# Kernel optimization log

Measured on AMD Instinct MI355X. Metric: run time of the kernel, lower is better.

The kernel has to match this reference:

```python
import jax, jax.numpy as jnp
import numpy as np

B, S, H, QKV, NH, MLP = 4, 2048, 512, 512, 8, 2048
HD = QKV // NH
EPS = 1e-6


def _layernorm(x):
    # LayerNorm over last dim, no affine, eps=1e-6
    mu = jnp.mean(x, axis=-1, keepdims=True)
    var = jnp.mean(jnp.square(x - mu), axis=-1, keepdims=True)
    return (x - mu) * jax.lax.rsqrt(var + EPS)


def setup_inputs() -> dict:
    key = jax.random.key(0)
    ks = jax.random.split(key, 8)
    sc_in = 1.0 / np.sqrt(H)
    sc_qkv = 1.0 / np.sqrt(QKV)
    sc_mlp = 1.0 / np.sqrt(MLP)
    return {
        "input": jax.random.normal(ks[0], (B, S, H), dtype=jnp.float32),
        "mask": jnp.ones((B, S), dtype=jnp.float32),
        "Wq": jax.random.normal(ks[1], (H, QKV), dtype=jnp.float32) * sc_in,
        "Wk": jax.random.normal(ks[2], (H, QKV), dtype=jnp.float32) * sc_in,
        "Wv": jax.random.normal(ks[3], (H, QKV), dtype=jnp.float32) * sc_in,
        "Wo": jax.random.normal(ks[4], (QKV, H), dtype=jnp.float32) * sc_qkv,
        "W1": jax.random.normal(ks[5], (H, MLP), dtype=jnp.float32) * sc_in,
        "W2": jax.random.normal(ks[6], (MLP, H), dtype=jnp.float32) * sc_mlp,
    }


def reference(input, mask, Wq, Wk, Wv, Wo, W1, W2):
    # pre-mask + pre-norm
    x = input * mask[..., None]
    x = _layernorm(x)
    # qkv projections, split heads: [B,S,QKV] -> [B,NH,S,HD]
    def heads(t):
        return t.reshape(B, S, NH, HD).transpose(0, 2, 1, 3)
    q = heads(x @ Wq) * (1.0 / np.sqrt(HD))
    k = heads(x @ Wk)
    v = heads(x @ Wv)
    logits = jnp.einsum("bhqd,bhkd->bhqk", q, k)  # [B,NH,S,S]
    amask = mask[:, None, :, None]  # 'b q -> b 1 q 1'
    logits = logits + (-100000.0) * (1.0 - amask)
    att = jax.nn.softmax(logits, axis=-1)
    out = jnp.einsum("bhqk,bhkd->bhqd", att, v)
    out = out.transpose(0, 2, 1, 3).reshape(B, S, QKV)
    x = input + out @ Wo  # residual
    x = x * mask[..., None]
    y = _layernorm(x)
    ffn = jax.nn.gelu(y @ W1, approximate=False) @ W2
    return ffn + x
```

## Files before the change

### kernel.cpp

```cpp
#include <hip/hip_runtime.h>
#include <hip/hip_bf16.h>
#include <cmath>

typedef __attribute__((ext_vector_type(8))) short bf16x8;
typedef __attribute__((ext_vector_type(4))) short u16x4;
typedef __attribute__((ext_vector_type(4))) float f32x4;
typedef __attribute__((ext_vector_type(16))) float f32x16;
typedef unsigned short u16;
typedef unsigned int u32;

#define B_ 4
#define S_ 2048
#define H_ 512
#define NH_ 8
#define HD_ 64
#define MLP_ 2048
#define M_ (B_*S_)
#define LOG2E 1.44269504088896340736f

__device__ __forceinline__ float bf2f(u16 u){ u32 v=((u32)u)<<16; float f; __builtin_memcpy(&f,&v,4); return f; }
__device__ __forceinline__ u16 f2bf(float f){ u32 u; __builtin_memcpy(&u,&f,4); u32 r=(u+0x7fffu+((u>>16)&1u))>>16; return (u16)r; }
__device__ __forceinline__ u32 pk2(float lo, float hi2){
  __hip_bfloat162 t = __float22bfloat162_rn(make_float2(lo, hi2));
  u32 r; __builtin_memcpy(&r, &t, 4); return r;
}

__device__ __forceinline__ float xhalf_add(float x){
  float a = x, b = x;
  asm volatile("v_permlane32_swap_b32 %0, %1" : "+v"(a), "+v"(b));
  return a + b;
}

__device__ __forceinline__ float gelu_fast(float x){
  float arg = 2.30221265f*x + 0.10295034f*x*x*x;
  arg = fminf(fmaxf(arg, -30.0f), 30.0f);
  float e = __builtin_amdgcn_exp2f(arg);
  return x * e * __builtin_amdgcn_rcpf(1.0f + e);
}

__device__ __forceinline__ void gl16(const u16* g, u16* l) {
  __builtin_amdgcn_global_load_lds((const __attribute__((address_space(1))) u32*)(g),
                                   (__attribute__((address_space(3))) u32*)(l), 16, 0, 0);
}

__device__ __forceinline__ void swz_mn(int* mt, int* nt) {
  int lin = blockIdx.x + 64*blockIdx.y;
  int xcd = lin & 7, idx = lin >> 3;
  *mt = xcd*8 + (idx & 7);
  *nt = idx >> 3;
}

__device__ __forceinline__ void gemm_core(
    const u16* __restrict__ A, const u16* __restrict__ Bt,
    int lda, int ldb, int nkt, int m0, int n0,
    u16* As, u16* Bs, f32x4 (&acc)[4][4])
{
  const int tid = threadIdx.x;
  const int lane = tid & 63;
  const int w = tid >> 6;
  const int lr = lane & 15;
  const int g  = lane >> 4;
  const int wr = w >> 1, wc = w & 1;

  const int sr = lane >> 3;
  const int scol = ((lane & 7) ^ sr) << 3;

  int aoff[2][4], boff[2][4];
#pragma unroll
  for (int m = 0; m < 4; ++m) {
    int ra = wr*64 + m*16 + lr;
    int rb = wc*64 + m*16 + lr;
#pragma unroll
    for (int kk = 0; kk < 2; ++kk) {
      aoff[kk][m] = ra*64 + (((kk*4+g) ^ (ra&7))<<3);
      boff[kk][m] = rb*64 + (((kk*4+g) ^ (rb&7))<<3);
    }
  }
  const u16* Ap = A + (size_t)m0*lda;
  const u16* Bp = Bt + (size_t)n0*ldb;

#pragma unroll
  for (int c = 0; c < 4; ++c) {
    gl16(Ap + (size_t)(w*32 + c*8 + sr)*lda + scol, As + w*2048 + c*512);
    gl16(Bp + (size_t)(w*32 + c*8 + sr)*ldb + scol, Bs + w*2048 + c*512);
  }

  for (int kt = 0; kt < nkt; ++kt) {
    const int cb = (kt & 1) * 8192;
    if (kt + 1 < nkt) {
      const int k0 = (kt + 1) << 6;
      const int nb = ((kt + 1) & 1) * 8192;
#pragma unroll
      for (int c = 0; c < 4; ++c) {
        gl16(Ap + (size_t)(w*32 + c*8 + sr)*lda + k0 + scol, As + nb + w*2048 + c*512);
        gl16(Bp + (size_t)(w*32 + c*8 + sr)*ldb + k0 + scol, Bs + nb + w*2048 + c*512);
      }
      asm volatile("s_waitcnt vmcnt(8)" ::: "memory");
    } else {
      asm volatile("s_waitcnt vmcnt(0)" ::: "memory");
    }
    __builtin_amdgcn_s_barrier();

#pragma unroll
    for (int kk = 0; kk < 2; ++kk) {
      bf16x8 af[4], bfr[4];
#pragma unroll
      for (int m = 0; m < 4; ++m) {
        af[m]  = *(const bf16x8*)(As + cb + aoff[kk][m]);
        bfr[m] = *(const bf16x8*)(Bs + cb + boff[kk][m]);
      }
#pragma unroll
      for (int m = 0; m < 4; ++m) {
#pragma unroll
        for (int n = 0; n < 4; ++n) {
          acc[m][n] = __builtin_amdgcn_mfma_f32_16x16x32_bf16(af[m], bfr[n], acc[m][n], 0, 0, 0);
        }
      }
    }
    __builtin_amdgcn_s_barrier();
  }
}

__device__ __forceinline__ void gemm_core64(
    const u16* __restrict__ A, const u16* __restrict__ Bt,
    int lda, int ldb, int nkt, int m0, int n0,
    u16* As, u16* Bs, f32x4 (&acc)[2][4])
{
  const int tid = threadIdx.x;
  const int lane = tid & 63;
  const int w = tid >> 6;
  const int lr = lane & 15;
  const int g  = lane >> 4;

  const int sr = lane >> 3;
  const int scol = ((lane & 7) ^ sr) << 3;

  int aoff[2][2], boff[2][4];
#pragma unroll
  for (int m = 0; m < 2; ++m) {
    int ra = w*32 + m*16 + lr;
#pragma unroll
    for (int kk = 0; kk < 2; ++kk) aoff[kk][m] = ra*64 + (((kk*4+g) ^ (ra&7))<<3);
  }
#pragma unroll
  for (int n = 0; n < 4; ++n) {
    int rb = n*16 + lr;
#pragma unroll
    for (int kk = 0; kk < 2; ++kk) boff[kk][n] = rb*64 + (((kk*4+g) ^ (rb&7))<<3);
  }
  const u16* Ap = A + (size_t)m0*lda;
  const u16* Bp = Bt + (size_t)n0*ldb;

#pragma unroll
  for (int c = 0; c < 4; ++c)
    gl16(Ap + (size_t)(w*32 + c*8 + sr)*lda + scol, As + w*2048 + c*512);
#pragma unroll
  for (int c = 0; c < 2; ++c)
    gl16(Bp + (size_t)(w*16 + c*8 + sr)*ldb + scol, Bs + w*1024 + c*512);

  for (int kt = 0; kt < nkt; ++kt) {
    const int cbA = (kt & 1) * 8192;
    const int cbB = (kt & 1) * 4096;
    if (kt + 1 < nkt) {
      const int k0 = (kt + 1) << 6;
      const int nbA = ((kt + 1) & 1) * 8192;
      const int nbB = ((kt + 1) & 1) * 4096;
#pragma unroll
      for (int c = 0; c < 4; ++c)
        gl16(Ap + (size_t)(w*32 + c*8 + sr)*lda + k0 + scol, As + nbA + w*2048 + c*512);
#pragma unroll
      for (int c = 0; c < 2; ++c)
        gl16(Bp + (size_t)(w*16 + c*8 + sr)*ldb + k0 + scol, Bs + nbB + w*1024 + c*512);
      asm volatile("s_waitcnt vmcnt(6)" ::: "memory");
    } else {
      asm volatile("s_waitcnt vmcnt(0)" ::: "memory");
    }
    __builtin_amdgcn_s_barrier();

#pragma unroll
    for (int kk = 0; kk < 2; ++kk) {
      bf16x8 af[2], bfr[4];
#pragma unroll
      for (int m = 0; m < 2; ++m) af[m] = *(const bf16x8*)(As + cbA + aoff[kk][m]);
#pragma unroll
      for (int n = 0; n < 4; ++n) bfr[n] = *(const bf16x8*)(Bs + cbB + boff[kk][n]);
#pragma unroll
      for (int m = 0; m < 2; ++m) {
#pragma unroll
        for (int n = 0; n < 4; ++n) {
          acc[m][n] = __builtin_amdgcn_mfma_f32_16x16x32_bf16(af[m], bfr[n], acc[m][n], 0, 0, 0);
        }
      }
    }
    __builtin_amdgcn_s_barrier();
  }
}

__global__ __launch_bounds__(256,2) void k_qkv(
    const u16* __restrict__ xn, const u16* __restrict__ wqt,
    const u16* __restrict__ wkt, const u16* __restrict__ wvt,
    u16* __restrict__ q, u16* __restrict__ k, u16* __restrict__ vt)
{
  __shared__ u16 As[2*128*64], Bs[2*128*64];
  int mt, nt; swz_mn(&mt, &nt);
  int m0 = mt*128;
  int sel = nt >> 2;
  int n0 = (nt & 3)*128;
  const u16* Bt = sel==0 ? wqt : (sel==1 ? wkt : wvt);
  f32x4 acc[4][4] = {};
  gemm_core(xn, Bt, H_, H_, H_/64, m0, n0, As, Bs, acc);
  const int lane = threadIdx.x&63, w = threadIdx.x>>6;
  const int lr = lane&15, g = lane>>4, wr = w>>1, wc = w&1;
  if (sel == 2) {
#pragma unroll
    for (int m=0;m<4;++m) {
#pragma unroll
      for (int n=0;n<4;++n) {
        int rowb = m0 + wr*64 + m*16 + g*4;
        int col  = n0 + wc*64 + n*16 + lr;
        int b = rowb >> 11, s = rowb & 2047;
        int h = col >> 6, d = col & 63;
        u16x4 t;
#pragma unroll
        for (int r=0;r<4;++r) t[r] = (short)f2bf(acc[m][n][r]);
        *(u16x4*)(vt + ((size_t)((b*NH_ + h)*HD_ + d))*S_ + s) = t;
      }
    }
  } else {
    u16* O = sel==0 ? q : k;
#pragma unroll
    for (int m=0;m<4;++m) {
#pragma unroll
      for (int n=0;n<4;++n) {
#pragma unroll
        for (int r=0;r<4;++r) {
          int row = m0 + wr*64 + m*16 + g*4 + r;
          int col = n0 + wc*64 + n*16 + lr;
          O[(size_t)row*H_ + col] = f2bf(acc[m][n][r]);
        }
      }
    }
  }
}

template<int EPI>
__global__ __launch_bounds__(256,2) void k_gemm(
    const u16* __restrict__ A, const u16* __restrict__ Bt, void* __restrict__ Ov,
    const void* __restrict__ aux, const float* __restrict__ maskv,
    int N, int K)
{
  __shared__ u16 As[2*128*64], Bs[2*128*64];
  int mt, nt; swz_mn(&mt, &nt);
  int m0 = mt*128, n0 = nt*128;
  f32x4 acc[4][4] = {};
  gemm_core(A, Bt, K, K, K>>6, m0, n0, As, Bs, acc);
  const int lane = threadIdx.x&63, w = threadIdx.x>>6;
  const int lr = lane&15, g = lane>>4, wr = w>>1, wc = w&1;
#pragma unroll
  for (int m=0;m<4;++m) {
#pragma unroll
    for (int n=0;n<4;++n) {
#pragma unroll
      for (int r=0;r<4;++r) {
        int row = m0 + wr*64 + m*16 + g*4 + r;
        int col = n0 + wc*64 + n*16 + lr;
        float val = acc[m][n][r];
        if (EPI == 1) {
          ((u16*)Ov)[(size_t)row*N + col] = f2bf(gelu_fast(val));
        }
      }
    }
  }
}

template<int EPI>
__global__ __launch_bounds__(256,3) void k_gemm64(
    const u16* __restrict__ A, const u16* __restrict__ Bt, void* __restrict__ Ov,
    const void* __restrict__ aux, const float* __restrict__ maskv,
    int N, int K)
{
  __shared__ u16 As[2*128*64], Bs[2*64*64];
  int mt, nt; swz_mn(&mt, &nt);
  int m0 = mt*128, n0 = nt*64;
  f32x4 acc[2][4] = {};
  gemm_core64(A, Bt, K, K, K>>6, m0, n0, As, Bs, acc);
  const int lane = threadIdx.x&63, w = threadIdx.x>>6;
  const int lr = lane&15, g = lane>>4;
#pragma unroll
  for (int m=0;m<2;++m) {
#pragma unroll
    for (int n=0;n<4;++n) {
#pragma unroll
      for (int r=0;r<4;++r) {
        int row = m0 + w*32 + m*16 + g*4 + r;
        int col = n0 + n*16 + lr;
        float val = acc[m][n][r];
        if (EPI == 2) {
          float mv = maskv[row];
          val = (((const float*)aux)[(size_t)row*N + col] + val)*mv;
          ((u16*)Ov)[(size_t)row*N + col] = f2bf(val);
        } else if (EPI == 3) {
          val += bf2f(((const u16*)aux)[(size_t)row*N + col]);
          ((float*)Ov)[(size_t)row*N + col] = val;
        }
      }
    }
  }
}

__global__ __launch_bounds__(256) void k_lnb(const u16* __restrict__ in,
    u16* __restrict__ out)
{
  int row = blockIdx.x*4 + (threadIdx.x>>6);
  int lane = threadIdx.x & 63;
  bf16x8 d = *(const bf16x8*)(in + (size_t)row*H_ + lane*8);
  float x[8]; float s = 0.f, s2 = 0.f;
#pragma unroll
  for (int j=0;j<8;++j){ x[j] = bf2f((u16)d[j]); s += x[j]; s2 += x[j]*x[j]; }
#pragma unroll
  for (int m=1;m<32;m<<=1){ s += __shfl_xor(s,m); s2 += __shfl_xor(s2,m); }
  s = xhalf_add(s); s2 = xhalf_add(s2);
  float mu = s*(1.0f/H_);
  float var = s2*(1.0f/H_) - mu*mu;
  float inv = rsqrtf(var + 1e-6f);
  bf16x8 o;
#pragma unroll
  for (int j=0;j<8;++j) o[j] = (short)f2bf((x[j]-mu)*inv);
  *(bf16x8*)(out + (size_t)row*H_ + lane*8) = o;
}

__global__ __launch_bounds__(256) void k_pre(
    const float* __restrict__ Wq, const float* __restrict__ Wk,
    const float* __restrict__ Wv, const float* __restrict__ Wo,
    const float* __restrict__ W1, const float* __restrict__ W2,
    u16* __restrict__ wqt, u16* __restrict__ wkt, u16* __restrict__ wvt,
    u16* __restrict__ wot, u16* __restrict__ w1t, u16* __restrict__ w2t,
    const float* __restrict__ input, const float* __restrict__ mask,
    u16* __restrict__ xn)
{
  __shared__ u16 t[32][33];
  const int id = blockIdx.x;
  const int tx = threadIdx.x & 31, ty = threadIdx.x >> 5;

  if (id < 1024) {
    int z = id >> 8, tt = id & 255;
    const float* src = z==0?Wq : z==1?Wk : z==2?Wv : Wo;
    u16* dst = z==0?wqt : z==1?wkt : z==2?wvt : wot;
    float sc = (z==0) ? 0.125f*LOG2E : 1.0f;
    int c0 = (tt & 15)*32, r0 = (tt >> 4)*32;
#pragma unroll
    for (int i=0;i<32;i+=8) t[ty+i][tx] = f2bf(src[(size_t)(r0+ty+i)*512 + c0+tx]*sc);
    __syncthreads();
#pragma unroll
    for (int i=0;i<32;i+=8) dst[(size_t)(c0+ty+i)*512 + r0+tx] = t[tx][ty+i];
  } else if (id < 3072) {
    int z = (id-1024) >> 10, tt = (id-1024) & 1023;
    const float* src = z ? W2 : W1;
    u16* dst = z ? w2t : w1t;
    int R = z ? 2048 : 512;
    int C = z ? 512 : 2048;
    int a = tt & 63, bq = tt >> 6;
    int c0 = (z ? bq : a)*32;
    int r0 = (z ? a : bq)*32;
#pragma unroll
    for (int i=0;i<32;i+=8) t[ty+i][tx] = f2bf(src[(size_t)(r0+ty+i)*C + c0+tx]);
    __syncthreads();
#pragma unroll
    for (int i=0;i<32;i+=8) dst[(size_t)(c0+ty+i)*R + r0+tx] = t[tx][ty+i];
  } else {
    int row = (id-3072)*4 + (threadIdx.x>>6);
    int lane = threadIdx.x & 63;
    const f32x4* p = (const f32x4*)(input + (size_t)row*H_ + lane*8);
    f32x4 a = p[0], b = p[1];
    float mv = mask[row];
    float x[8]; float s = 0.f, s2 = 0.f;
#pragma unroll
    for (int j=0;j<4;++j){ x[j] = a[j]*mv; x[4+j] = b[j]*mv; }
#pragma unroll
    for (int j=0;j<8;++j){ s += x[j]; s2 += x[j]*x[j]; }
#pragma unroll
    for (int m=1;m<32;m<<=1){ s += __shfl_xor(s,m); s2 += __shfl_xor(s2,m); }
    s = xhalf_add(s); s2 = xhalf_add(s2);
    float mu = s*(1.0f/H_);
    float var = s2*(1.0f/H_) - mu*mu;
    float inv = rsqrtf(var + 1e-6f);
    bf16x8 o;
#pragma unroll
    for (int j=0;j<8;++j) o[j] = (short)f2bf((x[j]-mu)*inv);
    *(bf16x8*)(xn + (size_t)row*H_ + lane*8) = o;
  }
}

__global__ __launch_bounds__(256) void k_attn(
    const u16* __restrict__ q, const u16* __restrict__ kmat,
    const u16* __restrict__ vt, const float* __restrict__ mask,
    u16* __restrict__ o)
{
  __shared__ u16 Ks[2][64*64];
  __shared__ u16 Vs[2][64*64];
  __shared__ float bias[S_];
  __shared__ float lsums[4][32];

  const int tid = threadIdx.x;
  const int lane = tid & 63;
  const int w = tid >> 6;
  const int l31 = lane & 31;
  const int hi = lane >> 5;
  const int bh = blockIdx.y, b = bh >> 3, h = bh & 7;
  const int q0 = blockIdx.x * 128;

  const int sr = lane >> 3;
  const int sl = (lane & 7) ^ (sr & 7);
  const u16* ks0 = kmat + (size_t)(b*S_ + w*16 + sr)*H_ + h*HD_ + sl*8;
  const u16* ks1 = ks0 + (size_t)8*H_;
  const u16* vs0 = vt + ((size_t)bh*HD_ + w*16 + sr)*S_ + sl*8;
  const u16* vs1 = vs0 + (size_t)8*S_;

  {
    u16* kd = &Ks[0][0] + w*1024;
    u16* vd = &Vs[0][0] + w*1024;
    gl16(ks0, kd); gl16(ks1, kd + 512);
    gl16(vs0, vd); gl16(vs1, vd + 512);
  }

  for (int j = tid; j < S_; j += 256) bias[j] = -144269.5f * (1.0f - mask[b*S_ + j]);

  bf16x8 qf[4];
  {
    const u16* qp = q + (size_t)(b*S_ + q0 + w*32 + l31)*H_ + h*HD_ + hi*8;
#pragma unroll
    for (int ds = 0; ds < 4; ++ds) qf[ds] = *(const bf16x8*)(qp + ds*16);
  }

  f32x16 po0 = {}, po1 = {};
  float mreg = -1e30f, lsum = 0.f;

  __syncthreads();

  for (int jt = 0; jt < 32; ++jt) {
    const int buf = jt & 1;
    if (jt < 31) {
      const int j0 = (jt + 1) * 64;
      u16* kd = &Ks[buf ^ 1][0] + w*1024;
      u16* vd = &Vs[buf ^ 1][0] + w*1024;
      gl16(ks0 + (size_t)j0*H_, kd); gl16(ks1 + (size_t)j0*H_, kd + 512);
      gl16(vs0 + j0, vd);            gl16(vs1 + j0, vd + 512);
      asm volatile("s_waitcnt vmcnt(4)" ::: "memory");
    } else {
      asm volatile("s_waitcnt vmcnt(0)" ::: "memory");
    }
    __builtin_amdgcn_s_barrier();

    const u16* kt  = &Ks[buf][0];
    const u16* vtl = &Vs[buf][0];

    f32x16 s0, s1;
    const float* bp = &bias[jt*64 + hi*4];
#pragma unroll
    for (int kb = 0; kb < 2; ++kb) {
      f32x16 acc;
#pragma unroll
      for (int g2 = 0; g2 < 4; ++g2) {
        f32x4 b4 = *(const f32x4*)(bp + kb*32 + g2*8);
        acc[g2*4+0] = b4[0]; acc[g2*4+1] = b4[1];
        acc[g2*4+2] = b4[2]; acc[g2*4+3] = b4[3];
      }
      const int key = kb*32 + l31;
      const u16* kr = kt + key*64;
      __builtin_amdgcn_s_setprio(1);
#pragma unroll
      for (int ds = 0; ds < 4; ++ds) {
        bf16x8 kf = *(const bf16x8*)(kr + (((ds*2 + hi) ^ (key & 7)) << 3));
        acc = __builtin_amdgcn_mfma_f32_32x32x16_bf16(kf, qf[ds], acc, 0, 0, 0);
      }
      __builtin_amdgcn_s_setprio(0);
      if (kb == 0) s0 = acc; else s1 = acc;
    }

    float mx = fmaxf(s0[0], s1[0]);
#pragma unroll
    for (int r = 1; r < 16; ++r) mx = fmaxf(fmaxf(s0[r], s1[r]), mx);
    mx = fmaxf(mx, __shfl_xor(mx, 32));
    if (__any(mx > mreg + 8.0f)) {
      float mn = fmaxf(mreg, mx);
      float sc = __builtin_amdgcn_exp2f(mreg - mn);
      lsum *= sc;
#pragma unroll
      for (int r = 0; r < 16; ++r) { po0[r] *= sc; po1[r] *= sc; }
      mreg = mn;
    }
    float ps = 0.f;
#pragma unroll
    for (int r = 0; r < 16; ++r) { float p = __builtin_amdgcn_exp2f(s0[r]-mreg); s0[r] = p; ps += p; }
#pragma unroll
    for (int r = 0; r < 16; ++r) { float p = __builtin_amdgcn_exp2f(s1[r]-mreg); s1[r] = p; ps += p; }
    ps += __shfl_xor(ps, 32);
    lsum += ps;

#pragma unroll
    for (int kb = 0; kb < 2; ++kb) {
      const f32x16& sv = kb ? s1 : s0;
      u32 w01 = pk2(sv[0],  sv[1]);
      u32 w23 = pk2(sv[2],  sv[3]);
      u32 w45 = pk2(sv[4],  sv[5]);
      u32 w67 = pk2(sv[6],  sv[7]);
      asm volatile("v_permlane32_swap_b32 %0, %1" : "+v"(w01), "+v"(w45));
      asm volatile("v_permlane32_swap_b32 %0, %1" : "+v"(w23), "+v"(w67));
      u32 w89 = pk2(sv[8],  sv[9]);
      u32 wab = pk2(sv[10], sv[11]);
      u32 wcd = pk2(sv[12], sv[13]);
      u32 wef = pk2(sv[14], sv[15]);
      asm volatile("v_permlane32_swap_b32 %0, %1" : "+v"(w89), "+v"(wcd));
      asm volatile("v_permlane32_swap_b32 %0, %1" : "+v"(wab), "+v"(wef));
      union { u32 wrd[4]; bf16x8 v; } f0, f1;
      f0.wrd[0]=w01; f0.wrd[1]=w23; f0.wrd[2]=w45; f0.wrd[3]=w67;
      f1.wrd[0]=w89; f1.wrd[1]=wab; f1.wrd[2]=wcd; f1.wrd[3]=wef;
      __builtin_amdgcn_s_setprio(1);
#pragma unroll
      for (int ks = 0; ks < 2; ++ks) {
        bf16x8 pa = ks ? f1.v : f0.v;
#pragma unroll
        for (int nb = 0; nb < 2; ++nb) {
          int dd = nb*32 + l31;
          int slot = ((kb*4 + ks*2 + hi) ^ (dd & 7)) << 3;
          bf16x8 vf = *(const bf16x8*)(vtl + dd*64 + slot);
          if (nb == 0) po0 = __builtin_amdgcn_mfma_f32_32x32x16_bf16(pa, vf, po0, 0,0,0);
          else         po1 = __builtin_amdgcn_mfma_f32_32x32x16_bf16(pa, vf, po1, 0,0,0);
        }
      }
      __builtin_amdgcn_s_setprio(0);
    }
    __builtin_amdgcn_s_barrier();
  }

  if (hi == 0) lsums[w][l31] = lsum;
  f32x4 li[4];
#pragma unroll
  for (int g2i = 0; g2i < 4; ++g2i) {
    f32x4 t = *(const f32x4*)&lsums[w][g2i*8 + hi*4];
    li[g2i][0] = 1.0f/t[0]; li[g2i][1] = 1.0f/t[1];
    li[g2i][2] = 1.0f/t[2]; li[g2i][3] = 1.0f/t[3];
  }
  u16* op = o + (size_t)(b*S_ + q0 + w*32)*H_ + h*HD_;
#pragma unroll
  for (int nb = 0; nb < 2; ++nb) {
#pragma unroll
    for (int r = 0; r < 16; ++r) {
      int row = (r&3) + 8*(r>>2) + 4*hi;
      float val = (nb ? po1[r] : po0[r]) * li[r>>2][r&3];
      op[(size_t)row*H_ + nb*32 + l31] = f2bf(val);
    }
  }
}

extern "C" void kernel_launch(void* const* d_in, const int* in_sizes, int n_in,
                              void* d_out, int out_size, void* d_ws, size_t ws_size,
                              hipStream_t stream) {
  const float* input = (const float*)d_in[0];
  const float* mask  = (const float*)d_in[1];
  const float* Wq = (const float*)d_in[2];
  const float* Wk = (const float*)d_in[3];
  const float* Wv = (const float*)d_in[4];
  const float* Wo = (const float*)d_in[5];
  const float* W1 = (const float*)d_in[6];
  const float* W2 = (const float*)d_in[7];
  float* out = (float*)d_out;
  u16* ws = (u16*)d_ws;

  u16* wqt = ws;
  u16* wkt = wqt + 262144;
  u16* wvt = wkt + 262144;
  u16* wot = wvt + 262144;
  u16* w1t = wot + 262144;
  u16* w2t = w1t + 1048576;
  u16* xn  = w2t + 1048576;
  u16* q   = xn  + 4194304;
  u16* k   = q   + 4194304;
  u16* v   = k   + 4194304;
  u16* vt  = v   + 4194304;
  u16*   attn = xn;
  u16*   x2b  = q;
  u16*   y    = v;
  u16*   h1   = vt;

  dim3 blk(256);
  k_pre<<<dim3(5120), blk, 0, stream>>>(Wq, Wk, Wv, Wo, W1, W2,
                                        wqt, wkt, wvt, wot, w1t, w2t,
                                        input, mask, xn);
  k_qkv<<<dim3(64,12), blk, 0, stream>>>(xn, wqt, wkt, wvt, q, k, vt);
  k_attn<<<dim3(16,32), blk, 0, stream>>>(q, k, vt, mask, attn);
  k_gemm64<2><<<dim3(64,8), blk, 0, stream>>>(attn, wot, (void*)x2b, (const void*)input, mask, 512, 512);
  k_lnb<<<2048, blk, 0, stream>>>(x2b, y);
  k_gemm<1><<<dim3(64,16), blk, 0, stream>>>(y, w1t, (void*)h1, nullptr, nullptr, 2048, 512);
  k_gemm64<3><<<dim3(64,8), blk, 0, stream>>>(h1, w2t, (void*)out, (const void*)x2b, nullptr, 512, 2048);
}
```

Baseline: 165.2 us.

## Fold second LayerNorm into W1 GEMM via column-sum correction

```diff
diff --git a/kernel.cpp b/kernel.cpp
--- a/kernel.cpp
+++ b/kernel.cpp
@@ -250,22 +250,49 @@
     int N, int K)
 {
   __shared__ u16 As[2*128*64], Bs[2*128*64];
+  __shared__ float muv[128], invv[128];
   int mt, nt; swz_mn(&mt, &nt);
   int m0 = mt*128, n0 = nt*128;
+
+  if (EPI == 1) {
+    const int t = threadIdx.x;
+    const int rl = t >> 1;
+    const int hf = t & 1;
+    const u16* xr = A + (size_t)(m0 + rl)*K + hf*256;
+    float s = 0.f, s2 = 0.f;
+#pragma unroll
+    for (int j = 0; j < 32; ++j) {
+      bf16x8 d = *(const bf16x8*)(xr + j*8);
+#pragma unroll
+      for (int e = 0; e < 8; ++e) { float x = bf2f((u16)d[e]); s += x; s2 += x*x; }
+    }
+    s += __shfl_xor(s, 1); s2 += __shfl_xor(s2, 1);
+    if (hf == 0) {
+      float mu = s*(1.0f/H_);
+      muv[rl] = mu;
+      invv[rl] = rsqrtf(s2*(1.0f/H_) - mu*mu + 1e-6f);
+    }
+  }
+
   f32x4 acc[4][4] = {};
   gemm_core(A, Bt, K, K, K>>6, m0, n0, As, Bs, acc);
   const int lane = threadIdx.x&63, w = threadIdx.x>>6;
   const int lr = lane&15, g = lane>>4, wr = w>>1, wc = w&1;
-#pragma unroll
-  for (int m=0;m<4;++m) {
-#pragma unroll
-    for (int n=0;n<4;++n) {
+  if (EPI == 1) {
+    float csv[4];
+#pragma unroll
+    for (int n=0;n<4;++n) csv[n] = maskv[n0 + wc*64 + n*16 + lr];
+#pragma unroll
+    for (int m=0;m<4;++m) {
 #pragma unroll
       for (int r=0;r<4;++r) {
-        int row = m0 + wr*64 + m*16 + g*4 + r;
-        int col = n0 + wc*64 + n*16 + lr;
-        float val = acc[m][n][r];
-        if (EPI == 1) {
+        int rl = wr*64 + m*16 + g*4 + r;
+        float mu = muv[rl], inv = invv[rl];
+        int row = m0 + rl;
+#pragma unroll
+        for (int n=0;n<4;++n) {
+          int col = n0 + wc*64 + n*16 + lr;
+          float val = inv*(acc[m][n][r] - mu*csv[n]);
           ((u16*)Ov)[(size_t)row*N + col] = f2bf(gelu_fast(val));
         }
       }
@@ -308,27 +335,6 @@
   }
 }
 
-__global__ __launch_bounds__(256) void k_lnb(const u16* __restrict__ in,
-    u16* __restrict__ out)
-{
-  int row = blockIdx.x*4 + (threadIdx.x>>6);
-  int lane = threadIdx.x & 63;
-  bf16x8 d = *(const bf16x8*)(in + (size_t)row*H_ + lane*8);
-  float x[8]; float s = 0.f, s2 = 0.f;
-#pragma unroll
-  for (int j=0;j<8;++j){ x[j] = bf2f((u16)d[j]); s += x[j]; s2 += x[j]*x[j]; }
-#pragma unroll
-  for (int m=1;m<32;m<<=1){ s += __shfl_xor(s,m); s2 += __shfl_xor(s2,m); }
-  s = xhalf_add(s); s2 = xhalf_add(s2);
-  float mu = s*(1.0f/H_);
-  float var = s2*(1.0f/H_) - mu*mu;
-  float inv = rsqrtf(var + 1e-6f);
-  bf16x8 o;
-#pragma unroll
-  for (int j=0;j<8;++j) o[j] = (short)f2bf((x[j]-mu)*inv);
-  *(bf16x8*)(out + (size_t)row*H_ + lane*8) = o;
-}
-
 __global__ __launch_bounds__(256) void k_pre(
     const float* __restrict__ Wq, const float* __restrict__ Wk,
     const float* __restrict__ Wv, const float* __restrict__ Wo,
@@ -336,7 +342,7 @@
     u16* __restrict__ wqt, u16* __restrict__ wkt, u16* __restrict__ wvt,
     u16* __restrict__ wot, u16* __restrict__ w1t, u16* __restrict__ w2t,
     const float* __restrict__ input, const float* __restrict__ mask,
-    u16* __restrict__ xn)
+    u16* __restrict__ xn, float* __restrict__ cs1)
 {
   __shared__ u16 t[32][33];
   const int id = blockIdx.x;
@@ -367,7 +373,7 @@
     __syncthreads();
 #pragma unroll
     for (int i=0;i<32;i+=8) dst[(size_t)(c0+ty+i)*R + r0+tx] = t[tx][ty+i];
-  } else {
+  } else if (id < 5120) {
     int row = (id-3072)*4 + (threadIdx.x>>6);
     int lane = threadIdx.x & 63;
     const f32x4* p = (const f32x4*)(input + (size_t)row*H_ + lane*8);
@@ -388,6 +394,11 @@
 #pragma unroll
     for (int j=0;j<8;++j) o[j] = (short)f2bf((x[j]-mu)*inv);
     *(bf16x8*)(xn + (size_t)row*H_ + lane*8) = o;
+  } else {
+    int c = (id-5120)*256 + threadIdx.x;
+    float s = 0.f;
+    for (int k2 = 0; k2 < 512; ++k2) s += bf2f(f2bf(W1[(size_t)k2*MLP_ + c]));
+    cs1[c] = s;
   }
 }
 
@@ -580,17 +591,16 @@
   u16* vt  = v   + 4194304;
   u16*   attn = xn;
   u16*   x2b  = q;
-  u16*   y    = v;
   u16*   h1   = vt;
+  float* cs1  = (float*)v;
 
   dim3 blk(256);
-  k_pre<<<dim3(5120), blk, 0, stream>>>(Wq, Wk, Wv, Wo, W1, W2,
+  k_pre<<<dim3(5128), blk, 0, stream>>>(Wq, Wk, Wv, Wo, W1, W2,
                                         wqt, wkt, wvt, wot, w1t, w2t,
-                                        input, mask, xn);
+                                        input, mask, xn, cs1);
   k_qkv<<<dim3(64,12), blk, 0, stream>>>(xn, wqt, wkt, wvt, q, k, vt);
   k_attn<<<dim3(16,32), blk, 0, stream>>>(q, k, vt, mask, attn);
   k_gemm64<2><<<dim3(64,8), blk, 0, stream>>>(attn, wot, (void*)x2b, (const void*)input, mask, 512, 512);
-  k_lnb<<<2048, blk, 0, stream>>>(x2b, y);
-  k_gemm<1><<<dim3(64,16), blk, 0, stream>>>(y, w1t, (void*)h1, nullptr, nullptr, 2048, 512);
+  k_gemm<1><<<dim3(64,16), blk, 0, stream>>>(x2b, w1t, (void*)h1, nullptr, cs1, 2048, 512);
   k_gemm64<3><<<dim3(64,8), blk, 0, stream>>>(h1, w2t, (void*)out, (const void*)x2b, nullptr, 512, 2048);
 }
```

Result: slower. 201.7 us (+22.1%).
